# Kernel optimization log

Measured on AMD Instinct MI355X. Metric: run time of the kernel, lower is better.

Reference implementation:

```python
import jax, jax.numpy as jnp
import numpy as np


def setup_inputs() -> dict:
    key = jax.random.key(0)
    ks = jax.random.split(key, 5)
    B, S, D, U = 16, 4096, 256, 256
    scale = 1.0 / np.sqrt(D)
    return {
        "values": jax.random.normal(ks[0], (B, S, D), dtype=jnp.float32),
        "query": jax.random.normal(ks[1], (B, D), dtype=jnp.float32),
        "W1": jax.random.normal(ks[2], (D, U), dtype=jnp.float32) * scale,
        "b1": jnp.zeros((U,), dtype=jnp.float32),
        "W2": jax.random.normal(ks[3], (D, U), dtype=jnp.float32) * scale,
        "b2": jnp.zeros((U,), dtype=jnp.float32),
        "V": jax.random.normal(ks[4], (U, 1), dtype=jnp.float32) * (1.0 / np.sqrt(U)),
        "bV": jnp.zeros((1,), dtype=jnp.float32),
    }


def reference(values, query, W1, b1, W2, b2, V, bV):
    # values: [B, S, D], query: [B, D]
    proj_v = jnp.einsum("bsd,du->bsu", values, W1) + b1          # [B, S, U]
    proj_q = (query @ W2 + b2)[:, None, :]                        # [B, 1, U]
    score = jnp.tanh(proj_v + proj_q) @ V + bV                    # [B, S, 1]
    attention_weights = jax.nn.softmax(score, axis=1)             # [B, S, 1]
    context_vector = jnp.sum(attention_weights * values, axis=1)  # [B, D]
    return context_vector, attention_weights
```

## Files before the change

### kernel.cpp

```cpp
#include <hip/hip_runtime.h>
#include <hip/hip_bf16.h>

#define B 16
#define S 4096
#define D 256
#define U 256
#define ROWS 32
#define NCHK (S / ROWS)

typedef short short8 __attribute__((ext_vector_type(8)));
typedef float f32x4 __attribute__((ext_vector_type(4)));

__device__ __forceinline__ ushort f2bf(float f) {
    union { float f; uint u; } x{f};
    uint r = (x.u + 0x7fffu + ((x.u >> 16) & 1u)) >> 16;
    return (ushort)r;
}

__device__ __forceinline__ float fast_tanh(float x) {
    float e = __expf(2.0f * x);
    return 1.0f - 2.0f * __builtin_amdgcn_rcpf(e + 1.0f);
}

__global__ void ka_setup(const float* __restrict__ query, const float* __restrict__ W2,
                         const float* __restrict__ b2, const float* __restrict__ b1,
                         const float* __restrict__ W1, float* __restrict__ pqb,
                         ushort* __restrict__ W1p) {
    __shared__ float pp[4][U];
    int bid = blockIdx.x, t = threadIdx.x;
    if (bid < 16) {
        const float* qb = query + bid * D;
        int u0 = (t & 63) * 4, dc = t >> 6;
        float4 a = {0.f, 0.f, 0.f, 0.f};
#pragma unroll 16
        for (int i = 0; i < 64; ++i) {
            int d = dc * 64 + i;
            float qd = qb[d];
            float4 wv = *(const float4*)&W2[d * U + u0];
            a.x = fmaf(qd, wv.x, a.x);
            a.y = fmaf(qd, wv.y, a.y);
            a.z = fmaf(qd, wv.z, a.z);
            a.w = fmaf(qd, wv.w, a.w);
        }
        *(float4*)&pp[dc][u0] = a;
        __syncthreads();
        pqb[bid * U + t] = pp[0][t] + pp[1][t] + pp[2][t] + pp[3][t] + b2[t] + b1[t];
    } else {
        int kk = bid - 16;
        int l = t & 63, g = t >> 6;
        int colu0 = l & 15;
        int k0 = kk * 32 + (l >> 4) * 8;
#pragma unroll
        for (int i = 0; i < 4; ++i) {
            int nt = g * 4 + i;
            int colu = nt * 16 + colu0;
            ushort* dst = W1p + (((nt * 8) + kk) * 64 + l) * 8;
#pragma unroll
            for (int e = 0; e < 8; ++e) dst[e] = f2bf(W1[(k0 + e) * U + colu]);
        }
    }
}

__global__ __launch_bounds__(256, 6) void kb_scores(
    const float* __restrict__ values, const ushort* __restrict__ W1p,
    const float* __restrict__ pqb, const float* __restrict__ V,
    const float* __restrict__ bV, float* __restrict__ cstats,
    float* __restrict__ cpart, float* __restrict__ wout) {
    __shared__ ushort Alds[ROWS * 256];
    __shared__ float red[4][ROWS];
    __shared__ float wch[ROWS];
    const int bid = blockIdx.x;
    const int t = threadIdx.x;
    const int w = t >> 6, l = t & 63;
    char* lds = (char*)Alds;
    const int b = bid >> 7;
    const int s0 = (bid & 127) * ROWS;

    const float* src = values + ((size_t)(b * S + s0)) * D;
#pragma unroll
    for (int i = 0; i < 8; ++i) {
        int row = i * 4 + w;
        int col = l * 4;
        float4 v = *(const float4*)&src[row * 256 + col];
        ushort4 h;
        h.x = f2bf(v.x); h.y = f2bf(v.y); h.z = f2bf(v.z); h.w = f2bf(v.w);
        int byte = (row * 512 + col * 2) ^ ((row & 7) << 4);
        *(ushort4*)(lds + byte) = h;
    }
    __syncthreads();

    const int lrow = l & 15, lk = l >> 4;
    f32x4 acc[2][4];
#pragma unroll
    for (int mt = 0; mt < 2; ++mt)
#pragma unroll
        for (int nt = 0; nt < 4; ++nt) acc[mt][nt] = (f32x4){0.f, 0.f, 0.f, 0.f};

    for (int kk = 0; kk < 8; ++kk) {
        short8 afr[2], bfr[4];
#pragma unroll
        for (int mt = 0; mt < 2; ++mt) {
            int row = mt * 16 + lrow;
            int byte = (row * 512 + kk * 64 + lk * 16) ^ ((row & 7) << 4);
            afr[mt] = *(const short8*)(lds + byte);
        }
#pragma unroll
        for (int nt = 0; nt < 4; ++nt)
            bfr[nt] = *(const short8*)&W1p[((((w * 4 + nt) * 8) + kk) * 64 + l) * 8];
#pragma unroll
        for (int mt = 0; mt < 2; ++mt)
#pragma unroll
            for (int nt = 0; nt < 4; ++nt)
                acc[mt][nt] = __builtin_amdgcn_mfma_f32_16x16x32_bf16(
                    afr[mt], bfr[nt], acc[mt][nt], 0, 0, 0);
    }

    float bb[4], vv[4];
#pragma unroll
    for (int nt = 0; nt < 4; ++nt) {
        int u = (w * 4 + nt) * 16 + lrow;
        bb[nt] = pqb[b * U + u];
        vv[nt] = V[u];
    }
#pragma unroll
    for (int mt = 0; mt < 2; ++mt) {
#pragma unroll
        for (int r = 0; r < 4; ++r) {
            float s = 0.f;
#pragma unroll
            for (int nt = 0; nt < 4; ++nt)
                s += fast_tanh(acc[mt][nt][r] + bb[nt]) * vv[nt];
            s += __shfl_xor(s, 1);
            s += __shfl_xor(s, 2);
            s += __shfl_xor(s, 4);
            s += __shfl_xor(s, 8);
            if (lrow == 0) red[w][mt * 16 + lk * 4 + r] = s;
        }
    }
    __syncthreads();

    if (t < ROWS) {
        float s = red[0][t] + red[1][t] + red[2][t] + red[3][t] + bV[0];
        float m = s;
#pragma unroll
        for (int off = 16; off; off >>= 1) m = fmaxf(m, __shfl_xor(m, off));
        float z0 = __expf(s - m);
        wch[t] = z0;
        wout[b * S + s0 + t] = z0;
        float z = z0;
#pragma unroll
        for (int off = 16; off; off >>= 1) z += __shfl_xor(z, off);
        if (t == 0) {
            cstats[2 * bid] = m;
            cstats[2 * bid + 1] = z;
        }
    }
    __syncthreads();

    union { uint i; float f; } cv;
    float cacc = 0.f;
#pragma unroll 8
    for (int r = 0; r < ROWS; ++r) {
        int byte = (r * 512 + t * 2) ^ ((r & 7) << 4);
        ushort u = *(const ushort*)(lds + byte);
        cv.i = (uint)u << 16;
        cacc = fmaf(wch[r], cv.f, cacc);
    }
    cpart[(size_t)bid * D + t] = cacc;
}

__global__ void kc_final(const float* __restrict__ cstats, const float* __restrict__ cpart,
                         float* __restrict__ wout, float* __restrict__ ctx) {
    __shared__ float scl[NCHK];
    __shared__ float stats2[2];
    __shared__ float part[4][64];
    int b = blockIdx.x >> 2, q = blockIdx.x & 3;
    int t = threadIdx.x;

    if (t < 64) {
        float m1 = cstats[2 * (b * NCHK + t)];
        float z1 = cstats[2 * (b * NCHK + t) + 1];
        float m2 = cstats[2 * (b * NCHK + 64 + t)];
        float z2 = cstats[2 * (b * NCHK + 64 + t) + 1];
        float M = fmaxf(m1, m2);
#pragma unroll
        for (int off = 32; off; off >>= 1) M = fmaxf(M, __shfl_xor(M, off));
        float zz = z1 * __expf(m1 - M) + z2 * __expf(m2 - M);
#pragma unroll
        for (int off = 32; off; off >>= 1) zz += __shfl_xor(zz, off);
        if (t == 0) { stats2[0] = M; stats2[1] = zz; }
    }
    __syncthreads();
    float M = stats2[0];
    float invZ = 1.0f / stats2[1];
    if (t < NCHK) scl[t] = __expf(cstats[2 * (b * NCHK + t)] - M);
    __syncthreads();

    int tq = t >> 6, dl = t & 63;
    int d = q * 64 + dl;
    float acc = 0.f;
#pragma unroll
    for (int i = 0; i < 32; ++i) {
        int c = tq * 32 + i;
        acc = fmaf(scl[c], cpart[(size_t)(b * NCHK + c) * D + d], acc);
    }
    part[tq][dl] = acc;

#pragma unroll
    for (int i = 0; i < 4; ++i) {
        int ss = q * 1024 + i * 256 + t;
        wout[b * S + ss] *= scl[ss >> 5] * invZ;
    }
    __syncthreads();
    if (t < 64)
        ctx[b * D + q * 64 + t] =
            (part[0][t] + part[1][t] + part[2][t] + part[3][t]) * invZ;
}

extern "C" void kernel_launch(void* const* d_in, const int* in_sizes, int n_in,
                              void* d_out, int out_size, void* d_ws, size_t ws_size,
                              hipStream_t stream) {
    const float* values = (const float*)d_in[0];
    const float* query  = (const float*)d_in[1];
    const float* W1     = (const float*)d_in[2];
    const float* b1     = (const float*)d_in[3];
    const float* W2     = (const float*)d_in[4];
    const float* b2     = (const float*)d_in[5];
    const float* V      = (const float*)d_in[6];
    const float* bV     = (const float*)d_in[7];

    float* out  = (float*)d_out;
    float* ctx  = out;
    float* wout = out + B * D;

    float* ws     = (float*)d_ws;
    float* pqb    = ws;
    float* cstats = pqb + B * U;
    float* cpart  = cstats + 2 * B * NCHK;
    ushort* W1p   = (ushort*)(cpart + (size_t)B * NCHK * D);

    ka_setup<<<24, 256, 0, stream>>>(query, W2, b2, b1, W1, pqb, W1p);
    kb_scores<<<B * NCHK, 256, 0, stream>>>(values, W1p, pqb, V, bV,
                                            cstats, cpart, wout);
    kc_final<<<B * 4, 256, 0, stream>>>(cstats, cpart, wout, ctx);
}
```

Before: 48.85 us.

## Process four chunks per block with async global-to-LDS prefetch double buffering

```diff
diff --git a/kernel.cpp b/kernel.cpp
--- a/kernel.cpp
+++ b/kernel.cpp
@@ -6,7 +6,8 @@
 #define D 256
 #define U 256
 #define ROWS 32
-#define NCHK (S / ROWS)
+#define NCHK 128
+#define CPB 4
 
 typedef short short8 __attribute__((ext_vector_type(8)));
 typedef float f32x4 __attribute__((ext_vector_type(4)));
@@ -61,59 +62,20 @@
     }
 }
 
-__global__ __launch_bounds__(256, 6) void kb_scores(
+__global__ __launch_bounds__(256, 2) void kb_scores(
     const float* __restrict__ values, const ushort* __restrict__ W1p,
     const float* __restrict__ pqb, const float* __restrict__ V,
-    const float* __restrict__ bV, float* __restrict__ cstats,
-    float* __restrict__ cpart, float* __restrict__ wout) {
-    __shared__ ushort Alds[ROWS * 256];
+    const float* __restrict__ bV, float* __restrict__ scores,
+    float* __restrict__ cstats, float* __restrict__ cpart) {
+    __shared__ float f32t[ROWS * 256];
+    __shared__ ushort bft[2][ROWS * 256];
     __shared__ float red[4][ROWS];
     __shared__ float wch[ROWS];
-    const int bid = blockIdx.x;
     const int t = threadIdx.x;
     const int w = t >> 6, l = t & 63;
-    char* lds = (char*)Alds;
-    const int b = bid >> 7;
-    const int s0 = (bid & 127) * ROWS;
-
-    const float* src = values + ((size_t)(b * S + s0)) * D;
-#pragma unroll
-    for (int i = 0; i < 8; ++i) {
-        int row = i * 4 + w;
-        int col = l * 4;
-        float4 v = *(const float4*)&src[row * 256 + col];
-        ushort4 h;
-        h.x = f2bf(v.x); h.y = f2bf(v.y); h.z = f2bf(v.z); h.w = f2bf(v.w);
-        int byte = (row * 512 + col * 2) ^ ((row & 7) << 4);
-        *(ushort4*)(lds + byte) = h;
-    }
-    __syncthreads();
-
     const int lrow = l & 15, lk = l >> 4;
-    f32x4 acc[2][4];
-#pragma unroll
-    for (int mt = 0; mt < 2; ++mt)
-#pragma unroll
-        for (int nt = 0; nt < 4; ++nt) acc[mt][nt] = (f32x4){0.f, 0.f, 0.f, 0.f};
-
-    for (int kk = 0; kk < 8; ++kk) {
-        short8 afr[2], bfr[4];
-#pragma unroll
-        for (int mt = 0; mt < 2; ++mt) {
-            int row = mt * 16 + lrow;
-            int byte = (row * 512 + kk * 64 + lk * 16) ^ ((row & 7) << 4);
-            afr[mt] = *(const short8*)(lds + byte);
-        }
-#pragma unroll
-        for (int nt = 0; nt < 4; ++nt)
-            bfr[nt] = *(const short8*)&W1p[((((w * 4 + nt) * 8) + kk) * 64 + l) * 8];
-#pragma unroll
-        for (int mt = 0; mt < 2; ++mt)
-#pragma unroll
-            for (int nt = 0; nt < 4; ++nt)
-                acc[mt][nt] = __builtin_amdgcn_mfma_f32_16x16x32_bf16(
-                    afr[mt], bfr[nt], acc[mt][nt], 0, 0, 0);
-    }
+    const int chunk0 = blockIdx.x * CPB;
+    const int b = chunk0 >> 7;
 
     float bb[4], vv[4];
 #pragma unroll
@@ -122,55 +84,133 @@
         bb[nt] = pqb[b * U + u];
         vv[nt] = V[u];
     }
-#pragma unroll
-    for (int mt = 0; mt < 2; ++mt) {
-#pragma unroll
-        for (int r = 0; r < 4; ++r) {
-            float s = 0.f;
+    const float bV0 = bV[0];
+
+#define DMA_CHUNK(chunk)                                                          \
+    {                                                                             \
+        const float* vb = values + ((size_t)(b * S + ((chunk) & 127) * ROWS)) * D;\
+        _Pragma("unroll")                                                         \
+        for (int i = 0; i < 8; ++i) {                                             \
+            int r = w * 8 + i;                                                    \
+            const float* g = vb + r * 256 + ((l ^ (r & 7)) * 4);                  \
+            __builtin_amdgcn_global_load_lds(                                     \
+                (const __attribute__((address_space(1))) void*)g,                 \
+                (__attribute__((address_space(3))) void*)&f32t[r * 256],          \
+                16, 0, 0);                                                        \
+        }                                                                         \
+    }
+
+#define CONVERT_CHUNK(pb)                                                         \
+    {                                                                             \
+        _Pragma("unroll")                                                         \
+        for (int i = 0; i < 8; ++i) {                                             \
+            int r = w * 8 + i;                                                    \
+            float4 v = *(const float4*)((const char*)f32t + r * 1024 +            \
+                                        ((l * 16) ^ ((r & 7) << 4)));             \
+            ushort4 h;                                                            \
+            h.x = f2bf(v.x); h.y = f2bf(v.y); h.z = f2bf(v.z); h.w = f2bf(v.w);   \
+            *(ushort4*)((char*)bft[pb] + r * 512 + ((l * 8) ^ ((r & 7) << 4))) = h;\
+        }                                                                         \
+    }
+
+    DMA_CHUNK(chunk0);
+    asm volatile("s_waitcnt vmcnt(0)" ::: "memory");
+    __builtin_amdgcn_sched_barrier(0);
+    CONVERT_CHUNK(0);
+
+    for (int c = 0; c < CPB; ++c) {
+        const int chunk = chunk0 + c;
+        const int s0 = (chunk & 127) * ROWS;
+        const char* bfb = (const char*)bft[c & 1];
+        __syncthreads();
+
+        if (c + 1 < CPB) DMA_CHUNK(chunk + 1);
+
+        f32x4 acc[2][4];
+#pragma unroll
+        for (int mt = 0; mt < 2; ++mt)
+#pragma unroll
+            for (int nt = 0; nt < 4; ++nt) acc[mt][nt] = (f32x4){0.f, 0.f, 0.f, 0.f};
+
+#pragma unroll
+        for (int kk = 0; kk < 8; ++kk) {
+            short8 afr[2], bfr[4];
 #pragma unroll
             for (int nt = 0; nt < 4; ++nt)
-                s += fast_tanh(acc[mt][nt][r] + bb[nt]) * vv[nt];
-            s += __shfl_xor(s, 1);
-            s += __shfl_xor(s, 2);
-            s += __shfl_xor(s, 4);
-            s += __shfl_xor(s, 8);
-            if (lrow == 0) red[w][mt * 16 + lk * 4 + r] = s;
-        }
-    }
-    __syncthreads();
-
-    if (t < ROWS) {
-        float s = red[0][t] + red[1][t] + red[2][t] + red[3][t] + bV[0];
-        float m = s;
-#pragma unroll
-        for (int off = 16; off; off >>= 1) m = fmaxf(m, __shfl_xor(m, off));
-        float z0 = __expf(s - m);
-        wch[t] = z0;
-        wout[b * S + s0 + t] = z0;
-        float z = z0;
-#pragma unroll
-        for (int off = 16; off; off >>= 1) z += __shfl_xor(z, off);
-        if (t == 0) {
-            cstats[2 * bid] = m;
-            cstats[2 * bid + 1] = z;
-        }
-    }
-    __syncthreads();
-
-    union { uint i; float f; } cv;
-    float cacc = 0.f;
+                bfr[nt] = *(const short8*)&W1p[((((w * 4 + nt) * 8) + kk) * 64 + l) * 8];
+#pragma unroll
+            for (int mt = 0; mt < 2; ++mt) {
+                int row = mt * 16 + lrow;
+                int byte = row * 512 + ((kk * 64 + lk * 16) ^ ((row & 7) << 4));
+                afr[mt] = *(const short8*)(bfb + byte);
+            }
+#pragma unroll
+            for (int mt = 0; mt < 2; ++mt)
+#pragma unroll
+                for (int nt = 0; nt < 4; ++nt)
+                    acc[mt][nt] = __builtin_amdgcn_mfma_f32_16x16x32_bf16(
+                        afr[mt], bfr[nt], acc[mt][nt], 0, 0, 0);
+        }
+
+#pragma unroll
+        for (int mt = 0; mt < 2; ++mt) {
+#pragma unroll
+            for (int r = 0; r < 4; ++r) {
+                float s = 0.f;
+#pragma unroll
+                for (int nt = 0; nt < 4; ++nt)
+                    s += fast_tanh(acc[mt][nt][r] + bb[nt]) * vv[nt];
+                s += __shfl_xor(s, 1);
+                s += __shfl_xor(s, 2);
+                s += __shfl_xor(s, 4);
+                s += __shfl_xor(s, 8);
+                if (lrow == 0) red[w][mt * 16 + lk * 4 + r] = s;
+            }
+        }
+        __syncthreads();
+
+        if (t < ROWS) {
+            float s = red[0][t] + red[1][t] + red[2][t] + red[3][t] + bV0;
+            scores[b * S + s0 + t] = s;
+            float m = s;
+#pragma unroll
+            for (int off = 16; off; off >>= 1) m = fmaxf(m, __shfl_xor(m, off));
+            float z0 = __expf(s - m);
+            wch[t] = z0;
+            float z = z0;
+#pragma unroll
+            for (int off = 16; off; off >>= 1) z += __shfl_xor(z, off);
+            if (t == 0) {
+                cstats[2 * chunk] = m;
+                cstats[2 * chunk + 1] = z;
+            }
+        }
+        __syncthreads();
+
+        union { uint i; float f; } cv;
+        float cacc = 0.f;
 #pragma unroll 8
-    for (int r = 0; r < ROWS; ++r) {
-        int byte = (r * 512 + t * 2) ^ ((r & 7) << 4);
-        ushort u = *(const ushort*)(lds + byte);
-        cv.i = (uint)u << 16;
-        cacc = fmaf(wch[r], cv.f, cacc);
-    }
-    cpart[(size_t)bid * D + t] = cacc;
-}
-
-__global__ void kc_final(const float* __restrict__ cstats, const float* __restrict__ cpart,
-                         float* __restrict__ wout, float* __restrict__ ctx) {
+        for (int r = 0; r < ROWS; ++r) {
+            int byte = r * 512 + ((t * 2) ^ ((r & 7) << 4));
+            ushort u = *(const ushort*)(bfb + byte);
+            cv.i = (uint)u << 16;
+            cacc = fmaf(wch[r], cv.f, cacc);
+        }
+        cpart[(size_t)chunk * D + t] = cacc;
+
+        if (c + 1 < CPB) {
+            asm volatile("s_waitcnt vmcnt(0)" ::: "memory");
+            __builtin_amdgcn_sched_barrier(0);
+            CONVERT_CHUNK((c + 1) & 1);
+        }
+    }
+#undef DMA_CHUNK
+#undef CONVERT_CHUNK
+}
+
+__global__ void kc_final(const float* __restrict__ scores, const float* __restrict__ cstats,
+                         const float* __restrict__ cpart, float* __restrict__ wout,
+                         float* __restrict__ ctx) {
     __shared__ float scl[NCHK];
     __shared__ float stats2[2];
     __shared__ float part[4][64];
@@ -209,7 +249,7 @@
 #pragma unroll
     for (int i = 0; i < 4; ++i) {
         int ss = q * 1024 + i * 256 + t;
-        wout[b * S + ss] *= scl[ss >> 5] * invZ;
+        wout[b * S + ss] = __expf(scores[b * S + ss] - M) * invZ;
     }
     __syncthreads();
     if (t < 64)
@@ -235,12 +275,13 @@
 
     float* ws     = (float*)d_ws;
     float* pqb    = ws;
-    float* cstats = pqb + B * U;
+    float* scores = pqb + B * U;
+    float* cstats = scores + B * S;
     float* cpart  = cstats + 2 * B * NCHK;
     ushort* W1p   = (ushort*)(cpart + (size_t)B * NCHK * D);
 
     ka_setup<<<24, 256, 0, stream>>>(query, W2, b2, b1, W1, pqb, W1p);
-    kb_scores<<<B * NCHK, 256, 0, stream>>>(values, W1p, pqb, V, bV,
-                                            cstats, cpart, wout);
-    kc_final<<<B * 4, 256, 0, stream>>>(cstats, cpart, wout, ctx);
-}
+    kb_scores<<<B * NCHK / CPB, 256, 0, stream>>>(values, W1p, pqb, V, bV,
+                                                  scores, cstats, cpart);
+    kc_final<<<B * 4, 256, 0, stream>>>(scores, cstats, cpart, wout, ctx);
+}
```

After: 55.25 us. +13.1%, slower.
